# Kernel tuning notes

Measured on AMD Instinct MI355X. Metric: run time of the kernel, lower is better.

## Reference

```python
import jax, jax.numpy as jnp
import numpy as np

B, N, P, E = 64, 512, 256, 4096          # batch, nodes (stations), partition nodes, edges
NUM_NWP, LP, F = 8, 16, 32               # num_nwp, local_points, local_cnn_dims
NT, ED, H, W = 8, 8, 64, 8               # num_temp, edge_feature_dims, decf_mlp_hidden, weight_function_dim
G, RH = 64, 256                          # gnn_dim, readout_hid_dim
H1, Q = 128, 9                           # mlp_hid_dim1, num quantiles


def setup_inputs() -> dict:
    key = jax.random.key(0)
    ks = iter(jax.random.split(key, 40))
    def rn(shape, s=0.05):
        return jax.random.normal(next(ks), shape, dtype=jnp.float32) * s
    # one-hot incidence matrices: each edge has one left (partition) node and one right node
    lidx = jax.random.randint(next(ks), (E,), 0, P)
    ridx = jax.random.randint(next(ks), (E,), 0, N)
    linc = jnp.zeros((P, E), jnp.float32).at[lidx, jnp.arange(E)].set(1.0)
    rinc = jnp.zeros((E, N), jnp.float32).at[jnp.arange(E), ridx].set(1.0)
    inp = {
        "x1": jax.random.normal(next(ks), (B, NUM_NWP * N, LP), dtype=jnp.float32),
        "x2": jax.random.normal(next(ks), (B, NT), dtype=jnp.float32),
        # LocalConv1D grouped conv (torch OIW layout: [Cout, Cin/groups, K])
        "conv_w": rn((F * N, NUM_NWP, LP)), "conv_b": rn((F * N,)),
        # WDSGCN2 edge-weight MLP
        "k1_w": rn((H, ED)), "k1_b": rn((H,)),
        "k2_w": rn((H, NT)),
        "k3_w": rn((H, F)),
        "k4_w": rn((H, F)),
        "k5_w": rn((W, H)), "k5_b": rn((W,)),
        "gc_w": rn((G, F * W)), "gc_b": rn((G,)),
        # readout
        "r0_w": rn((RH, G * P)),
        "r1_w": rn((RH, NT)), "r1_b": rn((RH,)),
        "r2_w": rn((RH, P)),
        "r3_w": rn((P, RH)), "r3_b": rn((P,)),
        # SMlp (forward uses l1 -> ELU -> l3 only)
        "l1_w": rn((H1, NT + G)), "l1_b": rn((H1,)),
        "l3_w": rn((Q, H1)), "l3_b": rn((Q,)),
        # buffers
        "ef": jax.random.normal(next(ks), (E, ED + 1), dtype=jnp.float32),
        "linc": linc,
        "rinc": rinc,
        "cap_feature": jax.random.normal(next(ks), (P,), dtype=jnp.float32),
        "partition_idx": jnp.arange(P, dtype=jnp.int32) * (N // P),
    }
    return inp


def reference(x1, x2, conv_w, conv_b, k1_w, k1_b, k2_w, k3_w, k4_w, k5_w, k5_b,
              gc_w, gc_b, r0_w, r1_w, r1_b, r2_w, r3_w, r3_b,
              l1_w, l1_b, l3_w, l3_b, ef, linc, rinc, cap_feature, partition_idx):
    b = x1.shape[0]
    # --- LocalConv1D: grouped conv1d (valid padding, output length 1) + ReLU ---
    y = jax.lax.conv_general_dilated(x1, conv_w, (1,), 'VALID',
                                     dimension_numbers=('NCH', 'OIH', 'NCH'),
                                     feature_group_count=N)
    x = jax.nn.relu(y + conv_b[None, :, None]).reshape(b, N, F)      # [B,N,F]
    # --- WDSGCN2: per-edge weight kernel ---
    kern = ef[:, :-1] @ k1_w.T + k1_b                                # [E,H]
    kern = kern[None] + (x2 @ k2_w.T)[:, None, :]                    # [B,E,H]
    xp = x[:, partition_idx, :]                                      # [B,P,F]
    kern = kern + jnp.einsum('pe,bpf->bef', linc, xp) @ k3_w.T       # left-node feats
    rx = jnp.einsum('en,bnf->bef', rinc, x)                          # right-node feats [B,E,F]
    kern = kern + rx @ k4_w.T
    kern = jax.nn.relu(jax.nn.leaky_relu(kern, 0.02) @ k5_w.T + k5_b)  # [B,E,W]
    # --- message = kernel (outer) right-node features, aggregated by left incidence ---
    msg = kern[:, :, :, None] * rx[:, :, None, :]                    # [B,E,W,F]
    agg = jnp.einsum('pe,bewf->bpwf', linc, msg).reshape(b, P, W * F)
    yg = jax.nn.relu(agg @ gc_w.T + gc_b)                            # [B,P,G]
    # --- readout attention over partition nodes ---
    h = yg.reshape(b, -1) @ r0_w.T + (x2 @ r1_w.T + r1_b) + cap_feature @ r2_w.T
    wt = jax.nn.relu(jax.nn.leaky_relu(h, 0.01) @ r3_w.T + r3_b)     # [B,P]
    res = jnp.einsum('bp,bpg->bg', wt, yg)                           # [B,G]
    # --- SMlp head ---
    z = jnp.concatenate([res, x2], axis=1)
    z = jax.nn.elu(z @ l1_w.T + l1_b)
    return z @ l3_w.T + l3_b                                         # [B,Q]
```

## Files before the change

kernel.cpp:

```cpp
#include <hip/hip_runtime.h>
#include <math.h>

#define B_ 64
#define N_ 512
#define P_ 256
#define E_ 4096
#define F_ 32
#define H_ 64
#define W_ 8
#define G_ 64
#define RH_ 256

#define X_OFF   0
#define T4_OFF  (X_OFF + N_*B_*F_)
#define T3_OFF  (T4_OFF + N_*B_*H_)
#define KB_OFF  (T3_OFF + P_*B_*H_)
#define KW_OFF  (KB_OFF + E_*H_)
#define YG_OFF  (KW_OFF + E_*B_*W_)
#define HB_OFF  (YG_OFF + B_*P_*G_)
#define RES_OFF (HB_OFF + B_*RH_)
#define INT_OFF (RES_OFF + 4*B_*G_)

__global__ __launch_bounds__(256) void k_dc(
    const float* __restrict__ linc, const float* __restrict__ rinc,
    int* __restrict__ lidx, int* __restrict__ ridx,
    const float* __restrict__ x1, const float* __restrict__ conv_w,
    const float* __restrict__ conv_b, float* __restrict__ x) {
  __shared__ float wsm[32 * 132];
  __shared__ float xsm[8192];
  int blk = blockIdx.x, t = threadIdx.x;
  if (blk < 3072) {
    int i4 = blk * 256 + t;
    const int L4 = (P_ * E_) / 4;
    if (i4 < L4) {
      float4 v = ((const float4*)linc)[i4];
      int i = i4 * 4;
      int p = i >> 12, e = i & 4095;
      if (v.x != 0.0f) lidx[e]     = p;
      if (v.y != 0.0f) lidx[e + 1] = p;
      if (v.z != 0.0f) lidx[e + 2] = p;
      if (v.w != 0.0f) lidx[e + 3] = p;
    } else {
      int j4 = i4 - L4;
      float4 v = ((const float4*)rinc)[j4];
      int j = j4 * 4;
      int e = j >> 9, n = j & 511;
      if (v.x != 0.0f) ridx[e] = n;
      if (v.y != 0.0f) ridx[e] = n + 1;
      if (v.z != 0.0f) ridx[e] = n + 2;
      if (v.w != 0.0f) ridx[e] = n + 3;
    }
    return;
  }
  int n = blk - 3072;
  for (int i = t; i < 1024; i += 256) {
    int f = i >> 5, j = i & 31;
    ((float4*)wsm)[f * 33 + j] = ((const float4*)(conv_w + n * 4096))[i];
  }
  for (int i = t; i < 2048; i += 256) {
    int b = i >> 5, j = i & 31;
    ((float4*)xsm)[i] = ((const float4*)(x1 + b * 65536 + n * 128))[j];
  }
  __syncthreads();
  int f = t & 31, bq = t >> 5;
  float cb = conv_b[n * 32 + f];
  float acc[8];
#pragma unroll
  for (int bi = 0; bi < 8; bi++) acc[bi] = cb;
  const float4* wf4 = (const float4*)wsm + f * 33;
  const float4* xb4 = (const float4*)xsm + bq * 256;
#pragma unroll 4
  for (int k4 = 0; k4 < 32; k4++) {
    float4 wv = wf4[k4];
#pragma unroll
    for (int bi = 0; bi < 8; bi++) {
      float4 xv = xb4[bi * 32 + k4];
      acc[bi] += wv.x * xv.x + wv.y * xv.y + wv.z * xv.z + wv.w * xv.w;
    }
  }
#pragma unroll
  for (int bi = 0; bi < 8; bi++) {
    int b = bq * 8 + bi;
    x[n * 2048 + b * 32 + f] = fmaxf(acc[bi], 0.0f);
  }
}

__global__ __launch_bounds__(256) void k_prep(
    const float* __restrict__ x, const int* __restrict__ pidx,
    const float* __restrict__ k3_w, const float* __restrict__ k4_w,
    const float* __restrict__ x2, const float* __restrict__ k2_w,
    const float* __restrict__ ef, const float* __restrict__ k1_w,
    const float* __restrict__ k1_b,
    const float* __restrict__ r1_w, const float* __restrict__ r1_b,
    const float* __restrict__ r2_w, const float* __restrict__ cap,
    const int* __restrict__ lidx, const int* __restrict__ ridx,
    float* __restrict__ t4, float* __restrict__ t3, float* __restrict__ kb,
    float* __restrict__ hbuf, int* __restrict__ part_start,
    int2* __restrict__ pe2) {
  __shared__ float xsh[2048];
  __shared__ float wsh[64 * 36];
  __shared__ float x2s[512];
  __shared__ float k2s[512];
  __shared__ int cnt[256];
  __shared__ int buf[256];
  __shared__ int cur[256];
  int blk = blockIdx.x, t = threadIdx.x;
  if (blk < 768) {
    bool isT4 = blk < 512;
    int n = isT4 ? blk : pidx[blk - 512];
    const float* wmat = isT4 ? k4_w : k3_w;
    float* outp = isT4 ? (t4 + blk * 4096) : (t3 + (blk - 512) * 4096);
    for (int i = t; i < 512; i += 256) {
      ((float4*)xsh)[i] = ((const float4*)(x + n * 2048))[i];
      int h = i >> 3, j = i & 7;
      ((float4*)wsh)[h * 9 + j] = ((const float4*)wmat)[i];
    }
    if (isT4) {
      for (int i = t; i < 128; i += 256) {
        ((float4*)x2s)[i] = ((const float4*)x2)[i];
        ((float4*)k2s)[i] = ((const float4*)k2_w)[i];
      }
    }
    __syncthreads();
    int h = t & 63, bq = t >> 6;
    float wreg[32];
#pragma unroll
    for (int j = 0; j < 8; j++) {
      float4 v = ((float4*)wsh)[h * 9 + j];
      wreg[4 * j] = v.x; wreg[4 * j + 1] = v.y; wreg[4 * j + 2] = v.z; wreg[4 * j + 3] = v.w;
    }
    float w2[8];
    if (isT4) {
      float4 u = ((float4*)k2s)[h * 2], v = ((float4*)k2s)[h * 2 + 1];
      w2[0] = u.x; w2[1] = u.y; w2[2] = u.z; w2[3] = u.w;
      w2[4] = v.x; w2[5] = v.y; w2[6] = v.z; w2[7] = v.w;
    }
    for (int bi = 0; bi < 16; bi++) {
      int b = bq * 16 + bi;
      float acc = 0.0f;
#pragma unroll
      for (int j = 0; j < 8; j++) {
        float4 xv = ((float4*)xsh)[b * 8 + j];
        acc += xv.x * wreg[4 * j] + xv.y * wreg[4 * j + 1] +
               xv.z * wreg[4 * j + 2] + xv.w * wreg[4 * j + 3];
      }
      if (isT4) {
        float4 u = ((float4*)x2s)[b * 2], v = ((float4*)x2s)[b * 2 + 1];
        acc += u.x * w2[0] + u.y * w2[1] + u.z * w2[2] + u.w * w2[3] +
               v.x * w2[4] + v.y * w2[5] + v.z * w2[6] + v.w * w2[7];
      }
      outp[b * 64 + h] = acc;
    }
  } else if (blk < 1792) {
    int o = (blk - 768) * 256 + t;
    int e = o >> 6, h = o & 63;
    float acc = k1_b[h];
    const float* er = ef + e * 9;
    const float* kr = k1_w + h * 8;
#pragma unroll
    for (int d = 0; d < 8; d++) acc += er[d] * kr[d];
    kb[o] = acc;
  } else if (blk < 1856) {
    int o = (blk - 1792) * 256 + t;
    int rh = o & 255;
    float acc = r1_b[rh];
    const float* xr = x2 + (o >> 8) * 8;
    const float* rr = r1_w + rh * 8;
#pragma unroll
    for (int d = 0; d < 8; d++) acc += xr[d] * rr[d];
    const float* r2r = r2_w + rh * 256;
    for (int p4 = 0; p4 < 64; p4++) {
      float4 cv = ((const float4*)cap)[p4];
      float4 rv = ((const float4*)r2r)[p4];
      acc += cv.x * rv.x + cv.y * rv.y + cv.z * rv.z + cv.w * rv.w;
    }
    hbuf[o] = acc;
  } else {
    cnt[t] = 0;
    __syncthreads();
    for (int e = t; e < E_; e += 256) atomicAdd(&cnt[lidx[e]], 1);
    __syncthreads();
    buf[t] = cnt[t];
    __syncthreads();
    for (int off = 1; off < 256; off <<= 1) {
      int add = (t >= off) ? buf[t - off] : 0;
      __syncthreads();
      buf[t] += add;
      __syncthreads();
    }
    part_start[t + 1] = buf[t];
    if (t == 0) part_start[0] = 0;
    cur[t] = buf[t] - cnt[t];
    __syncthreads();
    for (int e = t; e < E_; e += 256) {
      int p = lidx[e];
      int pos = atomicAdd(&cur[p], 1);
      pe2[pos] = make_int2(e, ridx[e]);
    }
  }
}

__global__ __launch_bounds__(512) void k_eagg(
    const float* __restrict__ x, const float* __restrict__ kb,
    const float* __restrict__ t3, const float* __restrict__ t4,
    const float* __restrict__ k5_w, const float* __restrict__ k5_b,
    const int2* __restrict__ pe2, const int* __restrict__ part_start,
    const float* __restrict__ gc_w, const float* __restrict__ gc_b,
    float* __restrict__ yg) {
  __shared__ float t3s[64 * 68];
  __shared__ float k5t[4 * 520];
  __shared__ float accS[64 * 128];
  int p = blockIdx.x, t = threadIdx.x;
  int slot = t >> 8;
  int ts = t & 255;
  int s = ts & 3, b = ts >> 2;
  {
    int h = t >> 3, w = t & 7;
    float v = k5_w[w * 64 + h];
#pragma unroll
    for (int qq = 0; qq < 4; qq++) k5t[qq * 520 + t] = v;
  }
  for (int i4 = t; i4 < 1024; i4 += 512) {
    float4 v = ((const float4*)(t3 + p * 4096))[i4];
    *(float4*)(t3s + (i4 >> 4) * 68 + (i4 & 15) * 4) = v;
  }
  __syncthreads();
  const float* kq = k5t + s * 520 + s * 128;
  float kb5[8];
#pragma unroll
  for (int w = 0; w < 8; w++) kb5[w] = k5_b[w];
  const float4* t3p = (const float4*)(t3s + b * 68 + s * 16);
  float acc[64];
#pragma unroll
  for (int j = 0; j < 64; j++) acc[j] = 0.0f;
  int s0 = part_start[p], s1 = part_start[p + 1];
  int idx0 = s0 + slot;
  int2 c = make_int2(0, 0);
  if (idx0 < s1) c = pe2[idx0];
  for (int idx = idx0; idx < s1; idx += 2) {
    int n2 = idx + 2;
    int2 cn = (n2 < s1) ? pe2[n2] : c;
    int e = c.x, r = c.y;
    const float4* xp = (const float4*)(x + r * 2048 + b * 32 + s * 8);
    float4 xq0 = xp[0], xq1 = xp[1];
    const float4* kb4 = (const float4*)(kb + e * 64 + s * 16);
    const float4* t44 = (const float4*)(t4 + r * 4096 + b * 64 + s * 16);
    float lk[16];
#pragma unroll
    for (int j4 = 0; j4 < 4; j4++) {
      float4 a = kb4[j4], cc = t3p[j4], d = t44[j4];
      float v;
      v = a.x + cc.x + d.x; lk[j4 * 4 + 0] = v > 0.0f ? v : 0.02f * v;
      v = a.y + cc.y + d.y; lk[j4 * 4 + 1] = v > 0.0f ? v : 0.02f * v;
      v = a.z + cc.z + d.z; lk[j4 * 4 + 2] = v > 0.0f ? v : 0.02f * v;
      v = a.w + cc.w + d.w; lk[j4 * 4 + 3] = v > 0.0f ? v : 0.02f * v;
    }
    float pw[8] = {0, 0, 0, 0, 0, 0, 0, 0};
#pragma unroll
    for (int j = 0; j < 16; j++) {
      float4 u = *(const float4*)(kq + j * 8);
      float4 v = *(const float4*)(kq + j * 8 + 4);
      float l = lk[j];
      pw[0] += l * u.x; pw[1] += l * u.y; pw[2] += l * u.z; pw[3] += l * u.w;
      pw[4] += l * v.x; pw[5] += l * v.y; pw[6] += l * v.z; pw[7] += l * v.w;
    }
#pragma unroll
    for (int w = 0; w < 8; w++) {
      pw[w] += __shfl_xor(pw[w], 1);
      pw[w] += __shfl_xor(pw[w], 2);
    }
    float kv[8];
#pragma unroll
    for (int w = 0; w < 8; w++) kv[w] = fmaxf(pw[w] + kb5[w], 0.0f);
    float xa[8] = {xq0.x, xq0.y, xq0.z, xq0.w, xq1.x, xq1.y, xq1.z, xq1.w};
#pragma unroll
    for (int w = 0; w < 8; w++)
#pragma unroll
      for (int j = 0; j < 8; j++) acc[w * 8 + j] += kv[w] * xa[j];
    c = cn;
  }
  int gq = t >> 6, be = t & 63;
  const float* gwb = gc_w + gq * 8 * 256;
  float ac[8];
#pragma unroll
  for (int i = 0; i < 8; i++) ac[i] = 0.0f;
#pragma unroll
  for (int ph = 0; ph < 2; ph++) {
    if (ph) __syncthreads();
    if (slot == 0) {
#pragma unroll
      for (int w2 = 0; w2 < 4; w2++)
#pragma unroll
        for (int j4 = 0; j4 < 2; j4++) {
          int khalf4 = w2 * 8 + s * 2 + j4;
          int phys4 = (khalf4 & 24) | ((khalf4 ^ b) & 7);
          int j = (ph * 4 + w2) * 8 + j4 * 4;
          *(float4*)(accS + b * 128 + phys4 * 4) =
              make_float4(acc[j], acc[j + 1], acc[j + 2], acc[j + 3]);
        }
    }
    __syncthreads();
    if (slot == 1) {
#pragma unroll
      for (int w2 = 0; w2 < 4; w2++)
#pragma unroll
        for (int j4 = 0; j4 < 2; j4++) {
          int khalf4 = w2 * 8 + s * 2 + j4;
          int phys4 = (khalf4 & 24) | ((khalf4 ^ b) & 7);
          int j = (ph * 4 + w2) * 8 + j4 * 4;
          float4* ptr = (float4*)(accS + b * 128 + phys4 * 4);
          float4 o = *ptr;
          o.x += acc[j]; o.y += acc[j + 1]; o.z += acc[j + 2]; o.w += acc[j + 3];
          *ptr = o;
        }
    }
    __syncthreads();
    for (int k4h = 0; k4h < 32; k4h++) {
      int phys4 = (k4h & 24) | ((k4h ^ be) & 7);
      float4 av = *(const float4*)(accS + be * 128 + phys4 * 4);
      int w2 = k4h >> 3;
      int k4g = (ph * 4 + w2) * 8 + (k4h & 7);
#pragma unroll
      for (int i = 0; i < 8; i++) {
        float4 wv = *(const float4*)(gwb + i * 256 + k4g * 4);
        ac[i] += av.x * wv.x + av.y * wv.y + av.z * wv.z + av.w * wv.w;
      }
    }
  }
  float* yp = yg + be * 16384 + p * 64 + gq * 8;
#pragma unroll
  for (int i = 0; i < 8; i++)
    yp[i] = fmaxf(ac[i] + gc_b[gq * 8 + i], 0.0f);
}

__global__ __launch_bounds__(256) void k_r0(const float* __restrict__ yg,
    const float* __restrict__ r0_w, float* __restrict__ part) {
  __shared__ float ygs[64 * 68];
  __shared__ float wts[64 * 260];
  int kc = blockIdx.x, t = threadIdx.x;
  int k0 = kc * 64;
  {
    int c = t >> 4, rr = t & 15;
    for (int rd = 0; rd < 16; rd++) {
      int rh = rd * 16 + rr;
      float4 v = *(const float4*)(r0_w + rh * 16384 + k0 + c * 4);
      wts[(4 * c + 0) * 260 + rh] = v.x;
      wts[(4 * c + 1) * 260 + rh] = v.y;
      wts[(4 * c + 2) * 260 + rh] = v.z;
      wts[(4 * c + 3) * 260 + rh] = v.w;
    }
  }
  {
    int b = t >> 2, kq = t & 3;
    const float* src = yg + b * 16384 + k0 + kq * 16;
#pragma unroll
    for (int u = 0; u < 4; u++) {
      float4 v = *(const float4*)(src + u * 4);
      int kk = kq * 16 + u * 4;
      ygs[(kk + 0) * 68 + b] = v.x;
      ygs[(kk + 1) * 68 + b] = v.y;
      ygs[(kk + 2) * 68 + b] = v.z;
      ygs[(kk + 3) * 68 + b] = v.w;
    }
  }
  __syncthreads();
  int lane = t & 63, wv = t >> 6;
  int b8 = lane & 7, r8 = lane >> 3;
  const float* yp = ygs + b8 * 8;
  const float* wp = wts + wv * 64 + r8 * 8;
  float acc[8][8];
#pragma unroll
  for (int i = 0; i < 8; i++)
#pragma unroll
    for (int j = 0; j < 8; j++) acc[i][j] = 0.0f;
#pragma unroll 2
  for (int k = 0; k < 64; k++) {
    float4 ya = *(const float4*)(yp + k * 68);
    float4 yb = *(const float4*)(yp + k * 68 + 4);
    float4 wa = *(const float4*)(wp + k * 260);
    float4 wb = *(const float4*)(wp + k * 260 + 4);
    float yv[8] = {ya.x, ya.y, ya.z, ya.w, yb.x, yb.y, yb.z, yb.w};
    float wr[8] = {wa.x, wa.y, wa.z, wa.w, wb.x, wb.y, wb.z, wb.w};
#pragma unroll
    for (int i = 0; i < 8; i++)
#pragma unroll
      for (int j = 0; j < 8; j++) acc[i][j] += yv[i] * wr[j];
  }
  float* pb = part + kc * 16384 + wv * 64 + r8 * 8;
#pragma unroll
  for (int i = 0; i < 8; i++) {
    float4 s0 = make_float4(acc[i][0], acc[i][1], acc[i][2], acc[i][3]);
    float4 s1 = make_float4(acc[i][4], acc[i][5], acc[i][6], acc[i][7]);
    float* pp = pb + (b8 * 8 + i) * 256;
    *(float4*)pp = s0;
    *(float4*)(pp + 4) = s1;
  }
}

__global__ __launch_bounds__(256) void k_r0red(const float* __restrict__ part,
    float* __restrict__ hbuf) {
  int blk = blockIdx.x;
  int oq = blk & 63, kq = blk >> 6;
  int o = oq * 256 + threadIdx.x;
  float s = 0.0f;
  const float* pp = part + kq * 64 * 16384 + o;
#pragma unroll 8
  for (int kc = 0; kc < 64; kc++) s += pp[kc * 16384];
  atomicAdd(&hbuf[o], s);
}

__global__ __launch_bounds__(256) void k_wt_res(const float* __restrict__ hbuf,
    const float* __restrict__ r3_w, const float* __restrict__ r3_b,
    const float* __restrict__ yg, float* __restrict__ res4) {
  __shared__ float hs[256];
  __shared__ float wts[64];
  __shared__ float red[256];
  int blk = blockIdx.x;
  int bb = blk >> 2, pq = blk & 3;
  int t = threadIdx.x;
  float hv = hbuf[bb * 256 + t];
  hs[t] = hv > 0.0f ? hv : 0.01f * hv;
  __syncthreads();
  int pl = t >> 2, c = t & 3;
  int pp = pq * 64 + pl;
  const float4* wrow = (const float4*)(r3_w + pp * 256 + c * 64);
  const float4* h4 = (const float4*)(hs) + c * 16;
  float a = 0.0f;
#pragma unroll
  for (int j = 0; j < 16; j++) {
    float4 w4 = wrow[j], hh = h4[j];
    a += hh.x * w4.x + hh.y * w4.y + hh.z * w4.z + hh.w * w4.w;
  }
  a += __shfl_xor(a, 1);
  a += __shfl_xor(a, 2);
  if (c == 0) wts[pl] = fmaxf(a + r3_b[pp], 0.0f);
  __syncthreads();
  int g = t & 63, ch = t >> 6;
  float r = 0.0f;
  const float* ygp = yg + bb * 16384 + pq * 4096 + g;
#pragma unroll
  for (int pi = 0; pi < 16; pi++) {
    int pl2 = ch * 16 + pi;
    r += wts[pl2] * ygp[pl2 * 64];
  }
  red[t] = r;
  __syncthreads();
  if (t < 64)
    res4[pq * 4096 + bb * 64 + t] = red[t] + red[t + 64] + red[t + 128] + red[t + 192];
}

__global__ __launch_bounds__(128) void k_final(const float* __restrict__ res4,
    const float* __restrict__ x2, const float* __restrict__ l1_w,
    const float* __restrict__ l1_b, const float* __restrict__ l3_w,
    const float* __restrict__ l3_b, float* __restrict__ out) {
  __shared__ float zs[128];
  int bb = blockIdx.x, t = threadIdx.x;
  float acc = l1_b[t];
  const float* wrow = l1_w + t * 72;
  const float* rr = res4 + bb * 64;
#pragma unroll 8
  for (int j = 0; j < 64; j++) {
    float rv = rr[j] + rr[4096 + j] + rr[8192 + j] + rr[12288 + j];
    acc += rv * wrow[j];
  }
  const float* xr = x2 + bb * 8;
#pragma unroll
  for (int j = 0; j < 8; j++) acc += xr[j] * wrow[64 + j];
  zs[t] = acc > 0.0f ? acc : expm1f(acc);
  __syncthreads();
  if (t < 9) {
    float o = l3_b[t];
    const float* w3 = l3_w + t * 128;
    for (int j = 0; j < 128; j++) o += zs[j] * w3[j];
    out[bb * 9 + t] = o;
  }
}

extern "C" void kernel_launch(void* const* d_in, const int* in_sizes, int n_in,
                              void* d_out, int out_size, void* d_ws, size_t ws_size,
                              hipStream_t stream) {
  (void)in_sizes; (void)n_in; (void)out_size; (void)ws_size;
  const float* x1     = (const float*)d_in[0];
  const float* x2     = (const float*)d_in[1];
  const float* conv_w = (const float*)d_in[2];
  const float* conv_b = (const float*)d_in[3];
  const float* k1_w   = (const float*)d_in[4];
  const float* k1_b   = (const float*)d_in[5];
  const float* k2_w   = (const float*)d_in[6];
  const float* k3_w   = (const float*)d_in[7];
  const float* k4_w   = (const float*)d_in[8];
  const float* k5_w   = (const float*)d_in[9];
  const float* k5_b   = (const float*)d_in[10];
  const float* gc_w   = (const float*)d_in[11];
  const float* gc_b   = (const float*)d_in[12];
  const float* r0_w   = (const float*)d_in[13];
  const float* r1_w   = (const float*)d_in[14];
  const float* r1_b   = (const float*)d_in[15];
  const float* r2_w   = (const float*)d_in[16];
  const float* r3_w   = (const float*)d_in[17];
  const float* r3_b   = (const float*)d_in[18];
  const float* l1_w   = (const float*)d_in[19];
  const float* l1_b   = (const float*)d_in[20];
  const float* l3_w   = (const float*)d_in[21];
  const float* l3_b   = (const float*)d_in[22];
  const float* ef     = (const float*)d_in[23];
  const float* linc   = (const float*)d_in[24];
  const float* rinc   = (const float*)d_in[25];
  const float* cap    = (const float*)d_in[26];
  const int*   pidx   = (const int*)d_in[27];
  float* out = (float*)d_out;

  float* ws   = (float*)d_ws;
  float* xbuf = ws + X_OFF;
  float* t4   = ws + T4_OFF;
  float* t3   = ws + T3_OFF;
  float* kb   = ws + KB_OFF;
  float* yg   = ws + YG_OFF;
  float* hbuf = ws + HB_OFF;
  float* res4 = ws + RES_OFF;
  float* part = ws + X_OFF;
  int* ib = (int*)(ws + INT_OFF);
  int* lidx = ib;
  int* ridx = ib + 4096;
  int* part_start = ib + 8192;
  int2* pe2 = (int2*)(ib + 8704);

  hipLaunchKernelGGL(k_dc, dim3(3584), dim3(256), 0, stream,
                     linc, rinc, lidx, ridx, x1, conv_w, conv_b, xbuf);
  hipLaunchKernelGGL(k_prep, dim3(1857), dim3(256), 0, stream,
                     xbuf, pidx, k3_w, k4_w, x2, k2_w, ef, k1_w, k1_b,
                     r1_w, r1_b, r2_w, cap, lidx, ridx,
                     t4, t3, kb, hbuf, part_start, pe2);
  hipLaunchKernelGGL(k_eagg, dim3(256), dim3(512), 0, stream,
                     xbuf, kb, t3, t4, k5_w, k5_b, pe2, part_start,
                     gc_w, gc_b, yg);
  hipLaunchKernelGGL(k_r0, dim3(256), dim3(256), 0, stream, yg, r0_w, part);
  hipLaunchKernelGGL(k_r0red, dim3(256), dim3(256), 0, stream, part, hbuf);
  hipLaunchKernelGGL(k_wt_res, dim3(256), dim3(256), 0, stream, hbuf, r3_w, r3_b, yg, res4);
  hipLaunchKernelGGL(k_final, dim3(64), dim3(128), 0, stream,
                     res4, x2, l1_w, l1_b, l3_w, l3_b, out);
}
```

Baseline: 260.9 us.

## Split edge-kernel MLP into its own edge-parallel kernel before per-partition aggregation

The per-partition fused kernel, which computed the edge-weight MLP and aggregated messages together, is split in two. A new edge-parallel kernel (4096 blocks) computes the kernel weights for every edge and batch and writes them to a workspace buffer in partition-sorted order. The aggregation kernel then only reads those weights plus the node features, and stages gc_w in shared memory. This removes the load imbalance from partitions with many edges and raises parallelism, at the cost of an extra kernel launch and a global round trip of the E×B×W weights. The partition index is packed into the upper bits of the edge id.

```diff
diff --git a/kernel.cpp b/kernel.cpp
--- a/kernel.cpp
+++ b/kernel.cpp
@@ -195,92 +195,98 @@
     for (int e = t; e < E_; e += 256) {
       int p = lidx[e];
       int pos = atomicAdd(&cur[p], 1);
-      pe2[pos] = make_int2(e, ridx[e]);
-    }
-  }
-}
-
-__global__ __launch_bounds__(512) void k_eagg(
-    const float* __restrict__ x, const float* __restrict__ kb,
-    const float* __restrict__ t3, const float* __restrict__ t4,
-    const float* __restrict__ k5_w, const float* __restrict__ k5_b,
+      pe2[pos] = make_int2(e | (p << 16), ridx[e]);
+    }
+  }
+}
+
+__global__ __launch_bounds__(256) void k_kern(
+    const float* __restrict__ kb, const float* __restrict__ t3,
+    const float* __restrict__ t4, const float* __restrict__ k5_w,
+    const float* __restrict__ k5_b, const int2* __restrict__ pe2,
+    float* __restrict__ kv) {
+  __shared__ float k5t[4 * 520];
+  int bid = blockIdx.x;
+  int pos = (bid & 7) * 512 + (bid >> 3);
+  int t = threadIdx.x;
+  for (int i = t; i < 512; i += 256) {
+    int h = i >> 3, w = i & 7;
+    float v = k5_w[w * 64 + h];
+#pragma unroll
+    for (int qq = 0; qq < 4; qq++) k5t[qq * 520 + i] = v;
+  }
+  int2 c = pe2[pos];
+  int e = c.x & 0xffff, p = c.x >> 16, r = c.y;
+  int s = t & 3, b = t >> 2;
+  __syncthreads();
+  const float* kq = k5t + s * 520 + s * 128;
+  const float4* kb4 = (const float4*)(kb + e * 64 + s * 16);
+  const float4* t34 = (const float4*)(t3 + p * 4096 + b * 64 + s * 16);
+  const float4* t44 = (const float4*)(t4 + r * 4096 + b * 64 + s * 16);
+  float lk[16];
+#pragma unroll
+  for (int j4 = 0; j4 < 4; j4++) {
+    float4 a = kb4[j4], cc = t34[j4], d = t44[j4];
+    float v;
+    v = a.x + cc.x + d.x; lk[j4 * 4 + 0] = v > 0.0f ? v : 0.02f * v;
+    v = a.y + cc.y + d.y; lk[j4 * 4 + 1] = v > 0.0f ? v : 0.02f * v;
+    v = a.z + cc.z + d.z; lk[j4 * 4 + 2] = v > 0.0f ? v : 0.02f * v;
+    v = a.w + cc.w + d.w; lk[j4 * 4 + 3] = v > 0.0f ? v : 0.02f * v;
+  }
+  float pw[8] = {0, 0, 0, 0, 0, 0, 0, 0};
+#pragma unroll
+  for (int j = 0; j < 16; j++) {
+    float4 u = *(const float4*)(kq + j * 8);
+    float4 v = *(const float4*)(kq + j * 8 + 4);
+    float l = lk[j];
+    pw[0] += l * u.x; pw[1] += l * u.y; pw[2] += l * u.z; pw[3] += l * u.w;
+    pw[4] += l * v.x; pw[5] += l * v.y; pw[6] += l * v.z; pw[7] += l * v.w;
+  }
+#pragma unroll
+  for (int w = 0; w < 8; w++) {
+    pw[w] += __shfl_xor(pw[w], 1);
+    pw[w] += __shfl_xor(pw[w], 2);
+  }
+  float2 o;
+  o.x = fmaxf(pw[2 * s] + k5_b[2 * s], 0.0f);
+  o.y = fmaxf(pw[2 * s + 1] + k5_b[2 * s + 1], 0.0f);
+  *(float2*)(kv + pos * 512 + b * 8 + 2 * s) = o;
+}
+
+__global__ __launch_bounds__(512, 2) void k_agg(
+    const float* __restrict__ x, const float* __restrict__ kv,
     const int2* __restrict__ pe2, const int* __restrict__ part_start,
     const float* __restrict__ gc_w, const float* __restrict__ gc_b,
     float* __restrict__ yg) {
-  __shared__ float t3s[64 * 68];
-  __shared__ float k5t[4 * 520];
   __shared__ float accS[64 * 128];
+  __shared__ float gcS[64 * 256];
   int p = blockIdx.x, t = threadIdx.x;
   int slot = t >> 8;
   int ts = t & 255;
   int s = ts & 3, b = ts >> 2;
-  {
-    int h = t >> 3, w = t & 7;
-    float v = k5_w[w * 64 + h];
-#pragma unroll
-    for (int qq = 0; qq < 4; qq++) k5t[qq * 520 + t] = v;
-  }
-  for (int i4 = t; i4 < 1024; i4 += 512) {
-    float4 v = ((const float4*)(t3 + p * 4096))[i4];
-    *(float4*)(t3s + (i4 >> 4) * 68 + (i4 & 15) * 4) = v;
-  }
-  __syncthreads();
-  const float* kq = k5t + s * 520 + s * 128;
-  float kb5[8];
-#pragma unroll
-  for (int w = 0; w < 8; w++) kb5[w] = k5_b[w];
-  const float4* t3p = (const float4*)(t3s + b * 68 + s * 16);
+  for (int i4 = t; i4 < 4096; i4 += 512)
+    ((float4*)gcS)[i4] = ((const float4*)gc_w)[i4];
   float acc[64];
 #pragma unroll
   for (int j = 0; j < 64; j++) acc[j] = 0.0f;
   int s0 = part_start[p], s1 = part_start[p + 1];
-  int idx0 = s0 + slot;
-  int2 c = make_int2(0, 0);
-  if (idx0 < s1) c = pe2[idx0];
-  for (int idx = idx0; idx < s1; idx += 2) {
-    int n2 = idx + 2;
-    int2 cn = (n2 < s1) ? pe2[n2] : c;
-    int e = c.x, r = c.y;
+  int idx = s0 + slot;
+  int r = (idx < s1) ? pe2[idx].y : 0;
+  for (; idx < s1; idx += 2) {
+    int rn = (idx + 2 < s1) ? pe2[idx + 2].y : 0;
+    const float4* kvp = (const float4*)(kv + idx * 512 + b * 8);
+    float4 ka = kvp[0], kc = kvp[1];
     const float4* xp = (const float4*)(x + r * 2048 + b * 32 + s * 8);
     float4 xq0 = xp[0], xq1 = xp[1];
-    const float4* kb4 = (const float4*)(kb + e * 64 + s * 16);
-    const float4* t44 = (const float4*)(t4 + r * 4096 + b * 64 + s * 16);
-    float lk[16];
-#pragma unroll
-    for (int j4 = 0; j4 < 4; j4++) {
-      float4 a = kb4[j4], cc = t3p[j4], d = t44[j4];
-      float v;
-      v = a.x + cc.x + d.x; lk[j4 * 4 + 0] = v > 0.0f ? v : 0.02f * v;
-      v = a.y + cc.y + d.y; lk[j4 * 4 + 1] = v > 0.0f ? v : 0.02f * v;
-      v = a.z + cc.z + d.z; lk[j4 * 4 + 2] = v > 0.0f ? v : 0.02f * v;
-      v = a.w + cc.w + d.w; lk[j4 * 4 + 3] = v > 0.0f ? v : 0.02f * v;
-    }
-    float pw[8] = {0, 0, 0, 0, 0, 0, 0, 0};
-#pragma unroll
-    for (int j = 0; j < 16; j++) {
-      float4 u = *(const float4*)(kq + j * 8);
-      float4 v = *(const float4*)(kq + j * 8 + 4);
-      float l = lk[j];
-      pw[0] += l * u.x; pw[1] += l * u.y; pw[2] += l * u.z; pw[3] += l * u.w;
-      pw[4] += l * v.x; pw[5] += l * v.y; pw[6] += l * v.z; pw[7] += l * v.w;
-    }
-#pragma unroll
-    for (int w = 0; w < 8; w++) {
-      pw[w] += __shfl_xor(pw[w], 1);
-      pw[w] += __shfl_xor(pw[w], 2);
-    }
-    float kv[8];
-#pragma unroll
-    for (int w = 0; w < 8; w++) kv[w] = fmaxf(pw[w] + kb5[w], 0.0f);
+    float kw[8] = {ka.x, ka.y, ka.z, ka.w, kc.x, kc.y, kc.z, kc.w};
     float xa[8] = {xq0.x, xq0.y, xq0.z, xq0.w, xq1.x, xq1.y, xq1.z, xq1.w};
 #pragma unroll
     for (int w = 0; w < 8; w++)
 #pragma unroll
-      for (int j = 0; j < 8; j++) acc[w * 8 + j] += kv[w] * xa[j];
-    c = cn;
+      for (int j = 0; j < 8; j++) acc[w * 8 + j] += kw[w] * xa[j];
+    r = rn;
   }
   int gq = t >> 6, be = t & 63;
-  const float* gwb = gc_w + gq * 8 * 256;
   float ac[8];
 #pragma unroll
   for (int i = 0; i < 8; i++) ac[i] = 0.0f;
@@ -322,7 +328,7 @@
       int k4g = (ph * 4 + w2) * 8 + (k4h & 7);
 #pragma unroll
       for (int i = 0; i < 8; i++) {
-        float4 wv = *(const float4*)(gwb + i * 256 + k4g * 4);
+        float4 wv = *(const float4*)(gcS + (gq * 8 + i) * 256 + k4g * 4);
         ac[i] += av.x * wv.x + av.y * wv.y + av.z * wv.z + av.w * wv.w;
       }
     }
@@ -515,6 +521,7 @@
   float* t4   = ws + T4_OFF;
   float* t3   = ws + T3_OFF;
   float* kb   = ws + KB_OFF;
+  float* kv   = ws + KW_OFF;
   float* yg   = ws + YG_OFF;
   float* hbuf = ws + HB_OFF;
   float* res4 = ws + RES_OFF;
@@ -531,9 +538,10 @@
                      xbuf, pidx, k3_w, k4_w, x2, k2_w, ef, k1_w, k1_b,
                      r1_w, r1_b, r2_w, cap, lidx, ridx,
                      t4, t3, kb, hbuf, part_start, pe2);
-  hipLaunchKernelGGL(k_eagg, dim3(256), dim3(512), 0, stream,
-                     xbuf, kb, t3, t4, k5_w, k5_b, pe2, part_start,
-                     gc_w, gc_b, yg);
+  hipLaunchKernelGGL(k_kern, dim3(4096), dim3(256), 0, stream,
+                     kb, t3, t4, k5_w, k5_b, pe2, kv);
+  hipLaunchKernelGGL(k_agg, dim3(256), dim3(512), 0, stream,
+                     xbuf, kv, pe2, part_start, gc_w, gc_b, yg);
   hipLaunchKernelGGL(k_r0, dim3(256), dim3(256), 0, stream, yg, r0_w, part);
   hipLaunchKernelGGL(k_r0red, dim3(256), dim3(256), 0, stream, part, hbuf);
   hipLaunchKernelGGL(k_wt_res, dim3(256), dim3(256), 0, stream, hbuf, r3_w, r3_b, yg, res4);
```

Result: faster. 240.7 us (-7.7%).
